# Kernel tuning notes

Hardware: AMD Instinct MI355X
Metric: run time of the kernel (lower is better)

The kernel has to match this reference:

```python
import jax, jax.numpy as jnp
import numpy as np

EPS = 1e-12
TOPK = 6

def _l2norm(x):
    # matches torch F.normalize(p=2, eps=1e-12)
    n = jnp.linalg.norm(x, axis=-1, keepdims=True)
    return x / jnp.maximum(n, EPS)

def setup_inputs() -> dict:
    key = jax.random.key(0)
    k1, k2 = jax.random.split(key)
    nC, M, P, d = 5, 512, 196, 384
    support = jax.random.normal(k1, (nC, P, d), dtype=jnp.float32)
    query = jax.random.normal(k2, (M, P, d), dtype=jnp.float32)
    scale_cls = jnp.full((1,), 10.0, dtype=jnp.float32)  # init value in module
    bias = jnp.zeros((1,), dtype=jnp.float32)
    return {"support": support, "query": query, "scale_cls": scale_cls, "bias": bias}

def reference(support, query, scale_cls, bias):
    q = _l2norm(query)      # [M, P, d]
    s = _l2norm(support)    # [nC, P, d]
    # batched cosine similarity between every query patch and support patch
    sim = jnp.einsum('mpd,cqd->mcpq', q, s)   # [M, nC, P, P]
    # max over support patches, then sum of top-6 query-patch matches
    m = sim.max(axis=3)                        # [M, nC, P]
    top6 = jax.lax.top_k(m, TOPK)[0].sum(axis=-1)  # [M, nC]
    cls_scores = top6[None]                    # [1, M, nC] (unsqueeze(0))
    return scale_cls * (cls_scores + bias)
```

## Files before the change

### kernel.cpp

```cpp
#include <hip/hip_runtime.h>
#include <hip/hip_bf16.h>
#include <cstdint>

typedef __attribute__((ext_vector_type(8))) short short8;
typedef __attribute__((ext_vector_type(4))) float floatx4;

#define NC   5
#define PP   196
#define DD   384
#define MM   512
#define ROWS (MM * PP)
#define NRB  1568
#define EPSN 1e-12f

#define TILE_BYTES  49152
#define KSTEP_BYTES 4096

__device__ __forceinline__ unsigned enc_f(float f) {
    unsigned u = __float_as_uint(f);
    return (u & 0x80000000u) ? ~u : (u | 0x80000000u);
}
__device__ __forceinline__ float dec_f(unsigned u) {
    unsigned b = (u & 0x80000000u) ? (u ^ 0x80000000u) : ~u;
    return __uint_as_float(b);
}
#define ENC_NEG_INF 0x007FFFFFu

__global__ __launch_bounds__(256) void k_norm0(const float* __restrict__ sup,
                                               float* __restrict__ sinv) {
    int wid = threadIdx.x >> 6, lane = threadIdx.x & 63;
    int r = blockIdx.x * 4 + wid;
    if (r >= NC * PP) return;
    const float* src = sup + (size_t)r * DD;
    float s = 0.f;
    #pragma unroll
    for (int j = 0; j < 6; ++j) { float v = src[lane + j * 64]; s += v * v; }
    #pragma unroll
    for (int off = 1; off < 64; off <<= 1) s += __shfl_xor(s, off, 64);
    if (lane == 0) sinv[r] = 1.0f / fmaxf(sqrtf(s), EPSN);
}

__global__ __launch_bounds__(256) void k_swz(const float* __restrict__ sup,
                                             const float* __restrict__ sinv,
                                             __hip_bfloat16* __restrict__ snw) {
    int s = blockIdx.x * 256 + threadIdx.x;
    int lane = s & 63;
    int r1 = s >> 6;
    int ct = r1 & 3;
    int r2 = r1 >> 2;
    int kk = r2 % 12;
    int g  = r2 / 12;
    int c = g >> 2, t = g & 3;
    int c16 = lane & 15, quad = lane >> 4;
    int cl = t * 64 + ct * 16 + c16;
    if (cl > PP - 1) cl = PP - 1;
    int srow = c * PP + cl;
    const float* sp = sup + (size_t)srow * DD + kk * 32 + quad * 8;
    float inv = sinv[srow];
    alignas(16) __hip_bfloat16 hb[8];
    #pragma unroll
    for (int e = 0; e < 8; ++e) hb[e] = __float2bfloat16(sp[e] * inv);
    *(uint4*)((char*)snw + (size_t)s * 16) = *(const uint4*)hb;
}

__global__ __launch_bounds__(256, 3) void k_gemm_max(const float* __restrict__ q,
                                                     const __hip_bfloat16* __restrict__ snw,
                                                     float* __restrict__ rowmaxg) {
    __shared__ __hip_bfloat16 As[12 * 4 * 64 * 8];
    __shared__ unsigned rmax[64 * NC];
    __shared__ float rss[64];

    const int tid  = threadIdx.x;
    const int row0 = blockIdx.x * 64;
    const int lane = tid & 63;
    const int wav  = tid >> 6;

    for (int i = tid; i < 64 * NC; i += 256) rmax[i] = ENC_NEG_INF;

    {
        const int arow = tid >> 2;
        const int asub = tid & 3;
        const int rt   = arow >> 4, c16 = arow & 15;
        const float* src = q + (size_t)(row0 + arow) * DD;
        float ss = 0.f;
        #pragma unroll
        for (int i = 0; i < 12; ++i) {
            int ch = asub + i * 4;
            const floatx4* p = (const floatx4*)(src + ch * 8);
            floatx4 x0 = __builtin_nontemporal_load(p);
            floatx4 x1 = __builtin_nontemporal_load(p + 1);
            ss += x0.x*x0.x + x0.y*x0.y + x0.z*x0.z + x0.w*x0.w
                + x1.x*x1.x + x1.y*x1.y + x1.z*x1.z + x1.w*x1.w;
            alignas(16) __hip_bfloat16 hb[8];
            hb[0] = __float2bfloat16(x0.x); hb[1] = __float2bfloat16(x0.y);
            hb[2] = __float2bfloat16(x0.z); hb[3] = __float2bfloat16(x0.w);
            hb[4] = __float2bfloat16(x1.x); hb[5] = __float2bfloat16(x1.y);
            hb[6] = __float2bfloat16(x1.z); hb[7] = __float2bfloat16(x1.w);
            int kk = ch >> 2, quad = ch & 3;
            *(uint4*)&As[(((kk * 4 + rt) * 64) + quad * 16 + c16) * 8] = *(const uint4*)hb;
        }
        ss += __shfl_xor(ss, 1, 64);
        ss += __shfl_xor(ss, 2, 64);
        if (asub == 0) rss[arow] = ss;
    }
    __syncthreads();

    const char* bbase = (const char*)snw + (size_t)wav * TILE_BYTES + (size_t)lane * 16;
    short8 b0[4], b1[4], b2[4], a[4];
    #pragma unroll
    for (int ct = 0; ct < 4; ++ct) b0[ct] = ((const short8*)(bbase + 0 * KSTEP_BYTES))[ct * 64];
    #pragma unroll
    for (int ct = 0; ct < 4; ++ct) b1[ct] = ((const short8*)(bbase + 1 * KSTEP_BYTES))[ct * 64];
    #pragma unroll
    for (int ct = 0; ct < 4; ++ct) b2[ct] = ((const short8*)(bbase + 2 * KSTEP_BYTES))[ct * 64];

    #define LOAD_NEXT(buf, step)                                                     \
        do {                                                                         \
            int nk = kk + 3 + (step);                                                \
            if (nk < 12) {                                                           \
                _Pragma("unroll")                                                    \
                for (int ct = 0; ct < 4; ++ct)                                       \
                    buf[ct] = ((const short8*)(bbase + nk * KSTEP_BYTES))[ct * 64];  \
            } else if (g + 4 < 20) {                                                 \
                _Pragma("unroll")                                                    \
                for (int ct = 0; ct < 4; ++ct)                                       \
                    buf[ct] = ((const short8*)(bbase + 4 * TILE_BYTES +              \
                                               (nk - 12) * KSTEP_BYTES))[ct * 64];   \
            }                                                                        \
        } while (0)

    #define MFMA_STEP(buf, kkoff)                                                    \
        do {                                                                         \
            _Pragma("unroll")                                                        \
            for (int rt = 0; rt < 4; ++rt)                                           \
                a[rt] = *(const short8*)&As[(((kk + (kkoff)) * 4 + rt) * 64 + lane) * 8]; \
            _Pragma("unroll")                                                        \
            for (int rt = 0; rt < 4; ++rt)                                           \
                _Pragma("unroll")                                                    \
                for (int ct = 0; ct < 4; ++ct)                                       \
                    acc[rt][ct] = __builtin_amdgcn_mfma_f32_16x16x32_bf16(           \
                        a[rt], buf[ct], acc[rt][ct], 0, 0, 0);                       \
        } while (0)

    #pragma unroll 1
    for (int g = wav; g < 20; g += 4) {
        floatx4 acc[4][4];
        #pragma unroll
        for (int i = 0; i < 4; ++i)
            #pragma unroll
            for (int j = 0; j < 4; ++j) acc[i][j] = (floatx4){0.f, 0.f, 0.f, 0.f};

        #pragma unroll 1
        for (int kk = 0; kk < 12; kk += 3) {
            MFMA_STEP(b0, 0); LOAD_NEXT(b0, 0);
            MFMA_STEP(b1, 1); LOAD_NEXT(b1, 1);
            MFMA_STEP(b2, 2); LOAD_NEXT(b2, 2);
        }

        const int c = g >> 2;
        const int quad = lane >> 4, c16 = lane & 15;
        #pragma unroll
        for (int rt = 0; rt < 4; ++rt) {
            #pragma unroll
            for (int reg = 0; reg < 4; ++reg) {
                float mx = fmaxf(fmaxf(acc[rt][0][reg], acc[rt][1][reg]),
                                 fmaxf(acc[rt][2][reg], acc[rt][3][reg]));
                #pragma unroll
                for (int off = 1; off < 16; off <<= 1)
                    mx = fmaxf(mx, __shfl_xor(mx, off, 64));
                if (c16 == 0) {
                    int rloc = rt * 16 + quad * 4 + reg;
                    atomicMax(&rmax[rloc * NC + c], enc_f(mx));
                }
            }
        }
        bbase += 4 * TILE_BYTES;
    }

    __syncthreads();
    for (int i = tid; i < 64 * NC; i += 256) {
        int c = i >> 6, row = i & 63;
        float inv = 1.0f / fmaxf(sqrtf(rss[row]), EPSN);
        __builtin_nontemporal_store(dec_f(rmax[row * NC + c]) * inv,
                                    &rowmaxg[(size_t)c * ROWS + row0 + row]);
    }
}

__global__ __launch_bounds__(256) void k_top6(const float* __restrict__ rowmaxg,
                                              const float* __restrict__ scale,
                                              const float* __restrict__ bias,
                                              float* __restrict__ out) {
    int wav = threadIdx.x >> 6, lane = threadIdx.x & 63;
    int pair = blockIdx.x * 4 + wav;
    if (pair >= MM * NC) return;
    int m = pair / NC, c = pair % NC;
    size_t base = (size_t)c * ROWS + (size_t)m * PP;
    float v[4];
    #pragma unroll
    for (int i = 0; i < 4; ++i) {
        int p = lane + i * 64;
        v[i] = (p < PP) ? rowmaxg[base + p] : -INFINITY;
    }
    float sum = 0.f;
    for (int t = 0; t < 6; ++t) {
        float bv = v[0]; int bi = 0;
        #pragma unroll
        for (int i = 1; i < 4; ++i) { if (v[i] > bv) { bv = v[i]; bi = i; } }
        int gid = bi * 64 + lane;
        #pragma unroll
        for (int off = 1; off < 64; off <<= 1) {
            float ov = __shfl_xor(bv, off, 64);
            int og  = __shfl_xor(gid, off, 64);
            if (ov > bv || (ov == bv && og < gid)) { bv = ov; gid = og; }
        }
        sum += bv;
        if ((gid & 63) == lane) v[gid >> 6] = -INFINITY;
    }
    if (lane == 0) out[pair] = scale[0] * (sum + bias[0]);
}

extern "C" void kernel_launch(void* const* d_in, const int* in_sizes, int n_in,
                              void* d_out, int out_size, void* d_ws, size_t ws_size,
                              hipStream_t stream) {
    const float* support = (const float*)d_in[0];
    const float* query   = (const float*)d_in[1];
    const float* scale   = (const float*)d_in[2];
    const float* bias    = (const float*)d_in[3];
    float* out = (float*)d_out;

    char* ws = (char*)d_ws;
    __hip_bfloat16* snw = (__hip_bfloat16*)ws;
    float* sinv         = (float*)(ws + 983040);
    float* rowmaxg      = (float*)(ws + 983040 + 4096);

    hipLaunchKernelGGL(k_norm0,   dim3(245),  dim3(256), 0, stream, support, sinv);
    hipLaunchKernelGGL(k_swz,     dim3(240),  dim3(256), 0, stream, support, sinv, snw);
    hipLaunchKernelGGL(k_gemm_max,dim3(NRB),  dim3(256), 0, stream, query, snw, rowmaxg);
    hipLaunchKernelGGL(k_top6,    dim3(640),  dim3(256), 0, stream, rowmaxg, scale, bias, out);
}
```

Before: 322.2 us.

## Pack support columns contiguously across classes and switch to 32x32x16 MFMA

Support patches are now laid out as one flat 980-column matrix in 16 tiles of 64 columns, replacing the per-class padded layout of 20 tiles. This cuts padded MFMA work by about a fifth. The GEMM moves from 16x16x32 to 32x32x16 bf16 MFMA with a 2x2 accumulator grid, and the row-max epilogue splits a tile's max by class when the tile straddles a class boundary. The initial B-fragment prefetch is also issued before the barrier. The cost is a more complex epilogue with extra shuffle passes on straddling tiles, and a different LDS access pattern.

```diff
diff --git a/kernel.cpp b/kernel.cpp
--- a/kernel.cpp
+++ b/kernel.cpp
@@ -4,6 +4,7 @@
 
 typedef __attribute__((ext_vector_type(8))) short short8;
 typedef __attribute__((ext_vector_type(4))) float floatx4;
+typedef __attribute__((ext_vector_type(16))) float floatx16;
 
 #define NC   5
 #define PP   196
@@ -13,8 +14,9 @@
 #define NRB  1568
 #define EPSN 1e-12f
 
+#define NTILES      16
 #define TILE_BYTES  49152
-#define KSTEP_BYTES 4096
+#define KSTEP_BYTES 2048
 
 __device__ __forceinline__ unsigned enc_f(float f) {
     unsigned u = __float_as_uint(f);
@@ -25,6 +27,10 @@
     return __uint_as_float(b);
 }
 #define ENC_NEG_INF 0x007FFFFFu
+
+__device__ __forceinline__ int cls_of(int col) {
+    return (col >= 784) ? 4 : (col >= 588) ? 3 : (col >= 392) ? 2 : (col >= 196) ? 1 : 0;
+}
 
 __global__ __launch_bounds__(256) void k_norm0(const float* __restrict__ sup,
                                                float* __restrict__ sinv) {
@@ -46,16 +52,14 @@
     int s = blockIdx.x * 256 + threadIdx.x;
     int lane = s & 63;
     int r1 = s >> 6;
-    int ct = r1 & 3;
-    int r2 = r1 >> 2;
-    int kk = r2 % 12;
-    int g  = r2 / 12;
-    int c = g >> 2, t = g & 3;
-    int c16 = lane & 15, quad = lane >> 4;
-    int cl = t * 64 + ct * 16 + c16;
-    if (cl > PP - 1) cl = PP - 1;
-    int srow = c * PP + cl;
-    const float* sp = sup + (size_t)srow * DD + kk * 32 + quad * 8;
+    int ct = r1 & 1;
+    int r2 = r1 >> 1;
+    int kk = r2 % 24;
+    int t  = r2 / 24;
+    int col = t * 64 + ct * 32 + (lane & 31);
+    if (col > NC * PP - 1) col = NC * PP - 1;
+    int srow = col;
+    const float* sp = sup + (size_t)srow * DD + kk * 16 + (lane >> 5) * 8;
     float inv = sinv[srow];
     alignas(16) __hip_bfloat16 hb[8];
     #pragma unroll
@@ -66,7 +70,7 @@
 __global__ __launch_bounds__(256, 3) void k_gemm_max(const float* __restrict__ q,
                                                      const __hip_bfloat16* __restrict__ snw,
                                                      float* __restrict__ rowmaxg) {
-    __shared__ __hip_bfloat16 As[12 * 4 * 64 * 8];
+    __shared__ __hip_bfloat16 As[24 * 2 * 64 * 8];
     __shared__ unsigned rmax[64 * NC];
     __shared__ float rss[64];
 
@@ -80,7 +84,7 @@
     {
         const int arow = tid >> 2;
         const int asub = tid & 3;
-        const int rt   = arow >> 4, c16 = arow & 15;
+        const int rt   = arow >> 5, r5 = arow & 31;
         const float* src = q + (size_t)(row0 + arow) * DD;
         float ss = 0.f;
         #pragma unroll
@@ -96,81 +100,114 @@
             hb[2] = __float2bfloat16(x0.z); hb[3] = __float2bfloat16(x0.w);
             hb[4] = __float2bfloat16(x1.x); hb[5] = __float2bfloat16(x1.y);
             hb[6] = __float2bfloat16(x1.z); hb[7] = __float2bfloat16(x1.w);
-            int kk = ch >> 2, quad = ch & 3;
-            *(uint4*)&As[(((kk * 4 + rt) * 64) + quad * 16 + c16) * 8] = *(const uint4*)hb;
+            int kk = ch >> 1, half = ch & 1;
+            *(uint4*)&As[((kk * 2 + rt) * 64 + half * 32 + r5) * 8] = *(const uint4*)hb;
         }
         ss += __shfl_xor(ss, 1, 64);
         ss += __shfl_xor(ss, 2, 64);
         if (asub == 0) rss[arow] = ss;
     }
+
+    const char* bbase = (const char*)snw + (size_t)wav * TILE_BYTES + (size_t)lane * 16;
+    short8 b0[2], b1[2], b2[2], a[2];
+    #pragma unroll
+    for (int ct = 0; ct < 2; ++ct) b0[ct] = ((const short8*)(bbase + 0 * KSTEP_BYTES))[ct * 64];
+    #pragma unroll
+    for (int ct = 0; ct < 2; ++ct) b1[ct] = ((const short8*)(bbase + 1 * KSTEP_BYTES))[ct * 64];
+    #pragma unroll
+    for (int ct = 0; ct < 2; ++ct) b2[ct] = ((const short8*)(bbase + 2 * KSTEP_BYTES))[ct * 64];
+
     __syncthreads();
-
-    const char* bbase = (const char*)snw + (size_t)wav * TILE_BYTES + (size_t)lane * 16;
-    short8 b0[4], b1[4], b2[4], a[4];
-    #pragma unroll
-    for (int ct = 0; ct < 4; ++ct) b0[ct] = ((const short8*)(bbase + 0 * KSTEP_BYTES))[ct * 64];
-    #pragma unroll
-    for (int ct = 0; ct < 4; ++ct) b1[ct] = ((const short8*)(bbase + 1 * KSTEP_BYTES))[ct * 64];
-    #pragma unroll
-    for (int ct = 0; ct < 4; ++ct) b2[ct] = ((const short8*)(bbase + 2 * KSTEP_BYTES))[ct * 64];
 
     #define LOAD_NEXT(buf, step)                                                     \
         do {                                                                         \
             int nk = kk + 3 + (step);                                                \
-            if (nk < 12) {                                                           \
+            if (nk < 24) {                                                           \
                 _Pragma("unroll")                                                    \
-                for (int ct = 0; ct < 4; ++ct)                                       \
+                for (int ct = 0; ct < 2; ++ct)                                       \
                     buf[ct] = ((const short8*)(bbase + nk * KSTEP_BYTES))[ct * 64];  \
-            } else if (g + 4 < 20) {                                                 \
+            } else if (g + 4 < NTILES) {                                             \
                 _Pragma("unroll")                                                    \
-                for (int ct = 0; ct < 4; ++ct)                                       \
+                for (int ct = 0; ct < 2; ++ct)                                       \
                     buf[ct] = ((const short8*)(bbase + 4 * TILE_BYTES +              \
-                                               (nk - 12) * KSTEP_BYTES))[ct * 64];   \
+                                               (nk - 24) * KSTEP_BYTES))[ct * 64];   \
             }                                                                        \
         } while (0)
 
     #define MFMA_STEP(buf, kkoff)                                                    \
         do {                                                                         \
             _Pragma("unroll")                                                        \
-            for (int rt = 0; rt < 4; ++rt)                                           \
-                a[rt] = *(const short8*)&As[(((kk + (kkoff)) * 4 + rt) * 64 + lane) * 8]; \
+            for (int rt = 0; rt < 2; ++rt)                                           \
+                a[rt] = *(const short8*)&As[(((kk + (kkoff)) * 2 + rt) * 64 + lane) * 8]; \
             _Pragma("unroll")                                                        \
-            for (int rt = 0; rt < 4; ++rt)                                           \
+            for (int rt = 0; rt < 2; ++rt)                                           \
                 _Pragma("unroll")                                                    \
-                for (int ct = 0; ct < 4; ++ct)                                       \
-                    acc[rt][ct] = __builtin_amdgcn_mfma_f32_16x16x32_bf16(           \
+                for (int ct = 0; ct < 2; ++ct)                                       \
+                    acc[rt][ct] = __builtin_amdgcn_mfma_f32_32x32x16_bf16(           \
                         a[rt], buf[ct], acc[rt][ct], 0, 0, 0);                       \
         } while (0)
 
     #pragma unroll 1
-    for (int g = wav; g < 20; g += 4) {
-        floatx4 acc[4][4];
-        #pragma unroll
-        for (int i = 0; i < 4; ++i)
+    for (int g = wav; g < NTILES; g += 4) {
+        floatx16 acc[2][2];
+        #pragma unroll
+        for (int i = 0; i < 2; ++i)
             #pragma unroll
-            for (int j = 0; j < 4; ++j) acc[i][j] = (floatx4){0.f, 0.f, 0.f, 0.f};
+            for (int j = 0; j < 2; ++j)
+                acc[i][j] = (floatx16){0.f,0.f,0.f,0.f, 0.f,0.f,0.f,0.f,
+                                       0.f,0.f,0.f,0.f, 0.f,0.f,0.f,0.f};
 
         #pragma unroll 1
-        for (int kk = 0; kk < 12; kk += 3) {
+        for (int kk = 0; kk < 24; kk += 3) {
             MFMA_STEP(b0, 0); LOAD_NEXT(b0, 0);
             MFMA_STEP(b1, 1); LOAD_NEXT(b1, 1);
             MFMA_STEP(b2, 2); LOAD_NEXT(b2, 2);
         }
 
-        const int c = g >> 2;
-        const int quad = lane >> 4, c16 = lane & 15;
-        #pragma unroll
-        for (int rt = 0; rt < 4; ++rt) {
+        {
+            const int colbase = g * 64;
+            int ce = colbase + 63; if (ce > NC * PP - 1) ce = NC * PP - 1;
+            const int clo = cls_of(colbase), chi = cls_of(ce);
+            int lcls[2];
             #pragma unroll
-            for (int reg = 0; reg < 4; ++reg) {
-                float mx = fmaxf(fmaxf(acc[rt][0][reg], acc[rt][1][reg]),
-                                 fmaxf(acc[rt][2][reg], acc[rt][3][reg]));
+            for (int ct = 0; ct < 2; ++ct) {
+                int col = colbase + ct * 32 + (lane & 31);
+                if (col > NC * PP - 1) col = NC * PP - 1;
+                lcls[ct] = cls_of(col);
+            }
+            const int hi = lane >> 5;
+            if (clo == chi) {
                 #pragma unroll
-                for (int off = 1; off < 16; off <<= 1)
-                    mx = fmaxf(mx, __shfl_xor(mx, off, 64));
-                if (c16 == 0) {
-                    int rloc = rt * 16 + quad * 4 + reg;
-                    atomicMax(&rmax[rloc * NC + c], enc_f(mx));
+                for (int rt = 0; rt < 2; ++rt)
+                    #pragma unroll
+                    for (int reg = 0; reg < 16; ++reg) {
+                        float v = fmaxf(acc[rt][0][reg], acc[rt][1][reg]);
+                        #pragma unroll
+                        for (int off = 1; off < 32; off <<= 1)
+                            v = fmaxf(v, __shfl_xor(v, off, 64));
+                        if ((lane & 31) == 0) {
+                            int row = rt * 32 + (reg & 3) + 8 * (reg >> 2) + 4 * hi;
+                            atomicMax(&rmax[row * NC + clo], enc_f(v));
+                        }
+                    }
+            } else {
+                #pragma unroll 1
+                for (int cc = clo; cc <= chi; ++cc) {
+                    #pragma unroll
+                    for (int rt = 0; rt < 2; ++rt)
+                        #pragma unroll
+                        for (int reg = 0; reg < 16; ++reg) {
+                            float v0 = (lcls[0] == cc) ? acc[rt][0][reg] : -INFINITY;
+                            float v1 = (lcls[1] == cc) ? acc[rt][1][reg] : -INFINITY;
+                            float v = fmaxf(v0, v1);
+                            #pragma unroll
+                            for (int off = 1; off < 32; off <<= 1)
+                                v = fmaxf(v, __shfl_xor(v, off, 64));
+                            if ((lane & 31) == 0) {
+                                int row = rt * 32 + (reg & 3) + 8 * (reg >> 2) + 4 * hi;
+                                atomicMax(&rmax[row * NC + cc], enc_f(v));
+                            }
+                        }
                 }
             }
         }
@@ -230,11 +267,11 @@
 
     char* ws = (char*)d_ws;
     __hip_bfloat16* snw = (__hip_bfloat16*)ws;
-    float* sinv         = (float*)(ws + 983040);
-    float* rowmaxg      = (float*)(ws + 983040 + 4096);
+    float* sinv         = (float*)(ws + 786432);
+    float* rowmaxg      = (float*)(ws + 786432 + 4096);
 
     hipLaunchKernelGGL(k_norm0,   dim3(245),  dim3(256), 0, stream, support, sinv);
-    hipLaunchKernelGGL(k_swz,     dim3(240),  dim3(256), 0, stream, support, sinv, snw);
+    hipLaunchKernelGGL(k_swz,     dim3(192),  dim3(256), 0, stream, support, sinv, snw);
     hipLaunchKernelGGL(k_gemm_max,dim3(NRB),  dim3(256), 0, stream, query, snw, rowmaxg);
     hipLaunchKernelGGL(k_top6,    dim3(640),  dim3(256), 0, stream, rowmaxg, scale, bias, out);
 }
```

Result: slower. 381.9 us (+18.5%).

## Pack support columns contiguously across classes to drop padding tiles

Applied to the files above, without the earlier changes.

Support patches are now laid out as one flat 980-column matrix split into 16 tiles of 64, instead of padding each class's 196 patches to 256 (20 tiles). Tiles that straddle a class boundary get a per-column class mask during the row-max reduction, with one reduction pass per class present. The barrier after staging A is also moved after the initial B register prefetch so that global loads overlap the barrier. This removes about a fifth of the MFMA work and B traffic, at the cost of extra reduction passes on the boundary tiles.

```diff
diff --git a/kernel.cpp b/kernel.cpp
--- a/kernel.cpp
+++ b/kernel.cpp
@@ -13,6 +13,7 @@
 #define NRB  1568
 #define EPSN 1e-12f
 
+#define NTILES      16
 #define TILE_BYTES  49152
 #define KSTEP_BYTES 4096
 
@@ -25,6 +26,10 @@
     return __uint_as_float(b);
 }
 #define ENC_NEG_INF 0x007FFFFFu
+
+__device__ __forceinline__ int cls_of(int col) {
+    return (col >= 784) ? 4 : (col >= 588) ? 3 : (col >= 392) ? 2 : (col >= 196) ? 1 : 0;
+}
 
 __global__ __launch_bounds__(256) void k_norm0(const float* __restrict__ sup,
                                                float* __restrict__ sinv) {
@@ -49,12 +54,11 @@
     int ct = r1 & 3;
     int r2 = r1 >> 2;
     int kk = r2 % 12;
-    int g  = r2 / 12;
-    int c = g >> 2, t = g & 3;
+    int t  = r2 / 12;
     int c16 = lane & 15, quad = lane >> 4;
-    int cl = t * 64 + ct * 16 + c16;
-    if (cl > PP - 1) cl = PP - 1;
-    int srow = c * PP + cl;
+    int col = t * 64 + ct * 16 + c16;
+    if (col > NC * PP - 1) col = NC * PP - 1;
+    int srow = col;
     const float* sp = sup + (size_t)srow * DD + kk * 32 + quad * 8;
     float inv = sinv[srow];
     alignas(16) __hip_bfloat16 hb[8];
@@ -103,7 +107,6 @@
         ss += __shfl_xor(ss, 2, 64);
         if (asub == 0) rss[arow] = ss;
     }
-    __syncthreads();
 
     const char* bbase = (const char*)snw + (size_t)wav * TILE_BYTES + (size_t)lane * 16;
     short8 b0[4], b1[4], b2[4], a[4];
@@ -113,6 +116,8 @@
     for (int ct = 0; ct < 4; ++ct) b1[ct] = ((const short8*)(bbase + 1 * KSTEP_BYTES))[ct * 64];
     #pragma unroll
     for (int ct = 0; ct < 4; ++ct) b2[ct] = ((const short8*)(bbase + 2 * KSTEP_BYTES))[ct * 64];
+
+    __syncthreads();
 
     #define LOAD_NEXT(buf, step)                                                     \
         do {                                                                         \
@@ -121,7 +126,7 @@
                 _Pragma("unroll")                                                    \
                 for (int ct = 0; ct < 4; ++ct)                                       \
                     buf[ct] = ((const short8*)(bbase + nk * KSTEP_BYTES))[ct * 64];  \
-            } else if (g + 4 < 20) {                                                 \
+            } else if (g + 4 < NTILES) {                                             \
                 _Pragma("unroll")                                                    \
                 for (int ct = 0; ct < 4; ++ct)                                       \
                     buf[ct] = ((const short8*)(bbase + 4 * TILE_BYTES +              \
@@ -143,7 +148,7 @@
         } while (0)
 
     #pragma unroll 1
-    for (int g = wav; g < 20; g += 4) {
+    for (int g = wav; g < NTILES; g += 4) {
         floatx4 acc[4][4];
         #pragma unroll
         for (int i = 0; i < 4; ++i)
@@ -157,20 +162,54 @@
             MFMA_STEP(b2, 2); LOAD_NEXT(b2, 2);
         }
 
-        const int c = g >> 2;
-        const int quad = lane >> 4, c16 = lane & 15;
-        #pragma unroll
-        for (int rt = 0; rt < 4; ++rt) {
-            #pragma unroll
-            for (int reg = 0; reg < 4; ++reg) {
-                float mx = fmaxf(fmaxf(acc[rt][0][reg], acc[rt][1][reg]),
-                                 fmaxf(acc[rt][2][reg], acc[rt][3][reg]));
+        {
+            const int colbase = g * 64;
+            int ce = colbase + 63; if (ce > NC * PP - 1) ce = NC * PP - 1;
+            const int clo = cls_of(colbase), chi = cls_of(ce);
+            const int quad = lane >> 4, c16 = lane & 15;
+            if (clo == chi) {
                 #pragma unroll
-                for (int off = 1; off < 16; off <<= 1)
-                    mx = fmaxf(mx, __shfl_xor(mx, off, 64));
-                if (c16 == 0) {
-                    int rloc = rt * 16 + quad * 4 + reg;
-                    atomicMax(&rmax[rloc * NC + c], enc_f(mx));
+                for (int rt = 0; rt < 4; ++rt) {
+                    #pragma unroll
+                    for (int reg = 0; reg < 4; ++reg) {
+                        float mx = fmaxf(fmaxf(acc[rt][0][reg], acc[rt][1][reg]),
+                                         fmaxf(acc[rt][2][reg], acc[rt][3][reg]));
+                        #pragma unroll
+                        for (int off = 1; off < 16; off <<= 1)
+                            mx = fmaxf(mx, __shfl_xor(mx, off, 64));
+                        if (c16 == 0) {
+                            int rloc = rt * 16 + quad * 4 + reg;
+                            atomicMax(&rmax[rloc * NC + clo], enc_f(mx));
+                        }
+                    }
+                }
+            } else {
+                int lcls[4];
+                #pragma unroll
+                for (int ct = 0; ct < 4; ++ct) {
+                    int col = colbase + ct * 16 + c16;
+                    if (col > NC * PP - 1) col = NC * PP - 1;
+                    lcls[ct] = cls_of(col);
+                }
+                #pragma unroll 1
+                for (int cc = clo; cc <= chi; ++cc) {
+                    #pragma unroll
+                    for (int rt = 0; rt < 4; ++rt) {
+                        #pragma unroll
+                        for (int reg = 0; reg < 4; ++reg) {
+                            float mx = -INFINITY;
+                            #pragma unroll
+                            for (int ct = 0; ct < 4; ++ct)
+                                if (lcls[ct] == cc) mx = fmaxf(mx, acc[rt][ct][reg]);
+                            #pragma unroll
+                            for (int off = 1; off < 16; off <<= 1)
+                                mx = fmaxf(mx, __shfl_xor(mx, off, 64));
+                            if (c16 == 0) {
+                                int rloc = rt * 16 + quad * 4 + reg;
+                                atomicMax(&rmax[rloc * NC + cc], enc_f(mx));
+                            }
+                        }
+                    }
                 }
             }
         }
@@ -230,11 +269,11 @@
 
     char* ws = (char*)d_ws;
     __hip_bfloat16* snw = (__hip_bfloat16*)ws;
-    float* sinv         = (float*)(ws + 983040);
-    float* rowmaxg      = (float*)(ws + 983040 + 4096);
+    float* sinv         = (float*)(ws + 786432);
+    float* rowmaxg      = (float*)(ws + 786432 + 4096);
 
     hipLaunchKernelGGL(k_norm0,   dim3(245),  dim3(256), 0, stream, support, sinv);
-    hipLaunchKernelGGL(k_swz,     dim3(240),  dim3(256), 0, stream, support, sinv, snw);
+    hipLaunchKernelGGL(k_swz,     dim3(192),  dim3(256), 0, stream, support, sinv, snw);
     hipLaunchKernelGGL(k_gemm_max,dim3(NRB),  dim3(256), 0, stream, query, snw, rowmaxg);
     hipLaunchKernelGGL(k_top6,    dim3(640),  dim3(256), 0, stream, rowmaxg, scale, bias, out);
 }
```

After: 312.8 us. 2.9% less time.
